# Kernel optimization log

Hardware: AMD Instinct MI355X
Metric: run time of the kernel (lower is better)

Reference implementation:

```python
import jax, jax.numpy as jnp
import numpy as np

N_HEAD = 16
D = 1024
LV = 2048
HEAD_DIM = D // N_HEAD
B = 2
LQ = 2048
LN_EPS = 1e-5


def setup_inputs() -> dict:
    key = jax.random.key(0)
    ks = jax.random.split(key, 8)
    s = 0.02
    v = jax.random.normal(ks[0], (B, LV, D), dtype=jnp.float32)
    q = jax.random.normal(ks[1], (B, LQ, D), dtype=jnp.float32)
    # per-head attn linear: d -> lv
    Wa = jax.random.normal(ks[2], (N_HEAD, D, LV), dtype=jnp.float32) * s
    ba = jnp.zeros((N_HEAD, LV), dtype=jnp.float32)
    # per-head layernorm over d
    gamma = jnp.ones((N_HEAD, D), dtype=jnp.float32)
    beta = jnp.zeros((N_HEAD, D), dtype=jnp.float32)
    # per-head proj (FilteredLinear modeled as affine): d -> head_dim
    Wp = jax.random.normal(ks[3], (N_HEAD, D, HEAD_DIM), dtype=jnp.float32) * s
    bp = jnp.zeros((N_HEAD, HEAD_DIM), dtype=jnp.float32)
    return {"v": v, "q": q, "Wa": Wa, "ba": ba, "gamma": gamma,
            "beta": beta, "Wp": Wp, "bp": bp}


def _mha(v, q, Wa, ba, gamma, beta, Wp, bp):
    # attn: [H, B, Lq, Lv] = relu(q @ Wa_h + ba_h)  (batched across heads)
    attn = jax.nn.relu(jnp.einsum('bqd,hdl->hbql', q, Wa)
                       + ba[:, None, None, :])
    # external-attention aggregation: [H, B, Lq, D]
    agg = jnp.einsum('hbql,bld->hbqd', attn, v)
    # per-head LayerNorm over last dim (d)
    mu = jnp.mean(agg, axis=-1, keepdims=True)
    var = jnp.var(agg, axis=-1, keepdims=True)
    normed = (agg - mu) * jax.lax.rsqrt(var + LN_EPS)
    normed = normed * gamma[:, None, None, :] + beta[:, None, None, :]
    # per-head projection to head_dim: [H, B, Lq, head_dim]
    heads = jnp.einsum('hbqd,hde->hbqe', normed, Wp) + bp[:, None, None, :]
    # concat heads along feature dim -> [B, Lq, D]
    return heads.transpose(1, 2, 0, 3).reshape(q.shape[0], q.shape[1], -1)


def reference(v, q, Wa, ba, gamma, beta, Wp, bp):
    return _mha(v, q, Wa, ba, gamma, beta, Wp, bp)
```

## Files before the change

### kernel.cpp

```cpp
#include <hip/hip_runtime.h>
#include <hip/hip_bf16.h>

typedef __attribute__((ext_vector_type(8))) short short8;
typedef __attribute__((ext_vector_type(4))) float f32x4;

#define N_HEAD 16
#define DMODEL 1024
#define LV 2048
#define LQ 2048
#define BATCH 2
#define HEAD_DIM 64

template <int N> struct IC { static constexpr int v = N; };

__device__ inline ushort f2bf(float f) {
    union { float f; unsigned u; } v; v.f = f;
    unsigned r = v.u + 0x7fffu + ((v.u >> 16) & 1u);
    return (ushort)(r >> 16);
}
__device__ inline float bf2f(ushort h) {
    union { unsigned u; float f; } v; v.u = ((unsigned)h) << 16;
    return v.f;
}

__global__ __launch_bounds__(256) void cast_bf16(const float* __restrict__ src,
                                                 ushort* __restrict__ dst, int n) {
    int i = (blockIdx.x * 256 + threadIdx.x) * 4;
    if (i < n) {
        float4 v = *(const float4*)(src + i);
        ushort4 o;
        o.x = f2bf(v.x); o.y = f2bf(v.y); o.z = f2bf(v.z); o.w = f2bf(v.w);
        *(ushort4*)(dst + i) = o;
    }
}

__global__ __launch_bounds__(256) void transpose_cast(const float* __restrict__ src,
                                                      ushort* __restrict__ dst,
                                                      int R, int C) {
    __shared__ float t[32][33];
    size_t zoff = (size_t)blockIdx.z * R * C;
    int c0 = blockIdx.x * 32, r0 = blockIdx.y * 32;
    int tx = threadIdx.x, ty = threadIdx.y;
#pragma unroll
    for (int i = 0; i < 4; ++i)
        t[ty + i * 8][tx] = src[zoff + (size_t)(r0 + ty + i * 8) * C + c0 + tx];
    __syncthreads();
#pragma unroll
    for (int i = 0; i < 4; ++i)
        dst[zoff + (size_t)(c0 + ty + i * 8) * R + r0 + tx] = f2bf(t[tx][ty + i * 8]);
}

template <bool RELU, int LNBN, int ZSH>
__global__ __launch_bounds__(512, 4) void gemm128x256(
    const ushort* __restrict__ A, const ushort* __restrict__ B,
    ushort* __restrict__ Cout, const float* __restrict__ bias,
    int K,
    long sA_b, long sA_h, long sB_b, long sB_h, long sC_z, int ldc, long sBias_h)
{
    __shared__ __align__(16) char smem[3 * 24576];

    const int gid = blockIdx.x;
    const int per = (int)gridDim.x >> 3;
    const int w = (gid & 7) * per + (gid >> 3);
    const int z = w >> ZSH;
    const int rem = w & ((1 << ZSH) - 1);
    const int bm0 = (rem >> LNBN) * 128;
    const int bn0 = (rem & ((1 << LNBN) - 1)) * 256;

    const int b = z & 1, h = z >> 1;
    A += (size_t)b * sA_b + (size_t)h * sA_h;
    B += (size_t)b * sB_b + (size_t)h * sB_h;
    const float* biasp = bias ? bias + (size_t)h * sBias_h : nullptr;

    const int T = threadIdx.x;
    const int lane = T & 63, wid = T >> 6;
    const int wr = wid >> 2, wc = wid & 3;
    const int fr = lane & 15, fq = lane >> 4;
    const int laneoff = fr * 64 + ((fq * 16) ^ ((fr >> 3) << 5));

    const int s_row = T >> 2;
    const int s_csw = ((T & 3) * 16) ^ (((T >> 5) & 1) << 5);
    const ushort* gA = A + (size_t)(bm0 + s_row) * K + (s_csw >> 1);
    const ushort* gB = B + (size_t)(bn0 + s_row) * K + (s_csw >> 1);

    const int nt = K >> 5;

    auto stage = [&](int sb, int kt) {
        char* base = smem + sb * 24576;
        const ushort* srcA = gA + (size_t)kt * 32;
        __builtin_amdgcn_global_load_lds(
            (const __attribute__((address_space(1))) void*)srcA,
            (__attribute__((address_space(3))) void*)(base + (T << 4)), 16, 0, 0);
#pragma unroll
        for (int j = 0; j < 2; ++j) {
            const ushort* srcB = gB + (size_t)j * 128 * K + (size_t)kt * 32;
            __builtin_amdgcn_global_load_lds(
                (const __attribute__((address_space(1))) void*)srcB,
                (__attribute__((address_space(3))) void*)(base + 8192 + j * 8192 + (T << 4)),
                16, 0, 0);
        }
    };

    f32x4 acc[4][4];
#pragma unroll
    for (int m = 0; m < 4; ++m)
#pragma unroll
        for (int n = 0; n < 4; ++n)
#pragma unroll
            for (int j = 0; j < 4; ++j) acc[m][n][j] = 0.f;

    auto step = [&](int t, int rb, int sb, auto DOST, auto VM) {
        const char* base = smem + rb * 24576;
        const char* pA = base + wr * 4096 + laneoff;
        const char* pB = base + 8192 + wc * 4096 + laneoff;
        short8 a[4], bb[4];
#pragma unroll
        for (int m = 0; m < 4; ++m) a[m] = *(const short8*)(pA + m * 1024);
#pragma unroll
        for (int n = 0; n < 4; ++n) bb[n] = *(const short8*)(pB + n * 1024);
        if constexpr (decltype(DOST)::v) stage(sb, t + 2);
        asm volatile("s_waitcnt lgkmcnt(0)" ::: "memory");
        __builtin_amdgcn_sched_barrier(0);
        __builtin_amdgcn_s_setprio(1);
#pragma unroll
        for (int m = 0; m < 4; ++m)
#pragma unroll
            for (int n = 0; n < 4; ++n)
                acc[m][n] = __builtin_amdgcn_mfma_f32_16x16x32_bf16(
                    a[m], bb[n], acc[m][n], 0, 0, 0);
        __builtin_amdgcn_s_setprio(0);
        __builtin_amdgcn_sched_barrier(0);
        constexpr int vm = decltype(VM)::v;
        if constexpr (vm == 3) asm volatile("s_waitcnt vmcnt(3)" ::: "memory");
        else if constexpr (vm == 0) asm volatile("s_waitcnt vmcnt(0)" ::: "memory");
        if constexpr (vm >= 0) asm volatile("s_barrier" ::: "memory");
    };

    stage(0, 0); stage(1, 1);
    asm volatile("s_waitcnt vmcnt(3)" ::: "memory");
    asm volatile("s_barrier" ::: "memory");

    int rb = 0, sb = 2;
    for (int t = 0; t < nt - 2; ++t) {
        step(t, rb, sb, IC<1>{}, IC<3>{});
        rb = (rb == 2) ? 0 : rb + 1;
        sb = (sb == 2) ? 0 : sb + 1;
    }
    step(nt - 2, rb, sb, IC<0>{}, IC<0>{});
    rb = (rb == 2) ? 0 : rb + 1;
    step(nt - 1, rb, sb, IC<0>{}, IC<-1>{});

    asm volatile("s_waitcnt vmcnt(0) lgkmcnt(0)" ::: "memory");
    __builtin_amdgcn_s_barrier();
    char* eb = smem + wid * 9216;
    const int row0 = bm0 + wr * 64;
    const int col0 = bn0 + wc * 64;
#pragma unroll
    for (int n = 0; n < 4; ++n) {
        const float bvv = biasp ? biasp[col0 + n * 16 + fr] : 0.f;
#pragma unroll
        for (int m = 0; m < 4; ++m) {
#pragma unroll
            for (int j = 0; j < 4; ++j) {
                float val = acc[m][n][j] + bvv;
                if (RELU) val = fmaxf(val, 0.f);
                *(ushort*)(eb + (m * 16 + fq * 4 + j) * 144 + (n * 16 + fr) * 2) = f2bf(val);
            }
        }
    }
    asm volatile("s_waitcnt lgkmcnt(0)" ::: "memory");
    ushort* C = Cout + (size_t)z * sC_z;
    const int rl = lane >> 3, cb = lane & 7;
#pragma unroll
    for (int i = 0; i < 8; ++i) {
        short8 vv = *(const short8*)(eb + (i * 8 + rl) * 144 + cb * 16);
        *(short8*)(C + (size_t)(row0 + i * 8 + rl) * ldc + col0 + cb * 8) = vv;
    }
}

__global__ __launch_bounds__(256) void lnproj_kernel(const ushort* __restrict__ agg,
                                                     const ushort* __restrict__ WpT,
                                                     const float* __restrict__ gamma,
                                                     const float* __restrict__ beta,
                                                     const float* __restrict__ bp,
                                                     float* __restrict__ out,
                                                     int h_base) {
    const int z = blockIdx.y, b = z & 1, hg = h_base + (z >> 1);
    const int wid = threadIdx.x >> 6, lane = threadIdx.x & 63;
    const int fr = lane & 15, fq = lane >> 4;
    const int m0 = (blockIdx.x * 4 + wid) * 16;

    const ushort* Arow = agg + ((size_t)z * 2048 + m0 + fr) * 1024 + fq * 8;

    float s = 0.f, s2 = 0.f;
    for (int kt = 0; kt < 32; ++kt) {
        short8 a = *(const short8*)(Arow + kt * 32);
#pragma unroll
        for (int j = 0; j < 8; ++j) { float x = bf2f((ushort)a[j]); s += x; s2 += x * x; }
    }
    s  += __shfl_xor(s, 16, 64);  s2 += __shfl_xor(s2, 16, 64);
    s  += __shfl_xor(s, 32, 64);  s2 += __shfl_xor(s2, 32, 64);
    const float mu  = s * (1.0f / 1024.0f);
    const float var = s2 * (1.0f / 1024.0f) - mu * mu;
    const float rs  = rsqrtf(fmaxf(var, 0.f) + 1e-5f);

    const ushort* Bbase = WpT + (size_t)hg * 64 * 1024 + (size_t)fr * 1024 + fq * 8;
    const float* gp = gamma + (size_t)hg * 1024 + fq * 8;
    const float* bt = beta  + (size_t)hg * 1024 + fq * 8;

    f32x4 acc[4];
#pragma unroll
    for (int n = 0; n < 4; ++n)
#pragma unroll
        for (int j = 0; j < 4; ++j) acc[n][j] = 0.f;

    for (int kt = 0; kt < 32; ++kt) {
        short8 a = *(const short8*)(Arow + kt * 32);
        float4 g0 = *(const float4*)(gp + kt * 32);
        float4 g1 = *(const float4*)(gp + kt * 32 + 4);
        float4 b0 = *(const float4*)(bt + kt * 32);
        float4 b1 = *(const float4*)(bt + kt * 32 + 4);
        const float gg[8] = {g0.x, g0.y, g0.z, g0.w, g1.x, g1.y, g1.z, g1.w};
        const float bb_[8] = {b0.x, b0.y, b0.z, b0.w, b1.x, b1.y, b1.z, b1.w};
        short8 an;
#pragma unroll
        for (int j = 0; j < 8; ++j) {
            float xn = (bf2f((ushort)a[j]) - mu) * rs * gg[j] + bb_[j];
            an[j] = (short)f2bf(xn);
        }
#pragma unroll
        for (int n = 0; n < 4; ++n) {
            short8 wv = *(const short8*)(Bbase + n * 16 * 1024 + kt * 32);
            acc[n] = __builtin_amdgcn_mfma_f32_16x16x32_bf16(an, wv, acc[n], 0, 0, 0);
        }
    }
#pragma unroll
    for (int n = 0; n < 4; ++n) {
        const int c = hg * 64 + n * 16 + fr;
        const float bvv = bp[c];
#pragma unroll
        for (int j = 0; j < 4; ++j)
            out[(size_t)b * 2048 * 1024 + (size_t)(m0 + fq * 4 + j) * 1024 + c] =
                acc[n][j] + bvv;
    }
}

extern "C" void kernel_launch(void* const* d_in, const int* in_sizes, int n_in,
                              void* d_out, int out_size, void* d_ws, size_t ws_size,
                              hipStream_t stream) {
    const float* v     = (const float*)d_in[0];
    const float* q     = (const float*)d_in[1];
    const float* Wa    = (const float*)d_in[2];
    const float* ba    = (const float*)d_in[3];
    const float* gamma = (const float*)d_in[4];
    const float* beta  = (const float*)d_in[5];
    const float* Wp    = (const float*)d_in[6];
    const float* bp    = (const float*)d_in[7];
    float* out = (float*)d_out;

    const size_t MB = 1ull << 20;
    char* ws = (char*)d_ws;
    ushort* qbf = (ushort*)(ws);
    ushort* vT  = (ushort*)(ws + 8 * MB);
    ushort* WpT = (ushort*)(ws + 16 * MB);
    int NH = 1;
    {
        const int cands[5] = {16, 8, 4, 2, 1};
        for (int i = 0; i < 5; ++i) {
            if ((size_t)(18 + 28 * cands[i]) * MB <= ws_size) { NH = cands[i]; break; }
        }
    }
    ushort* WaT_c  = (ushort*)(ws + 18 * MB);
    ushort* attn_c = (ushort*)(ws + (18 + (size_t)4 * NH) * MB);
    ushort* agg_c  = (ushort*)(ws + (18 + (size_t)20 * NH) * MB);

    dim3 tb(32, 8);
    cast_bf16<<<4096, 256, 0, stream>>>(q, qbf, BATCH * LQ * DMODEL);
    transpose_cast<<<dim3(DMODEL / 32, LV / 32, BATCH), tb, 0, stream>>>(v, vT, LV, DMODEL);
    transpose_cast<<<dim3(HEAD_DIM / 32, DMODEL / 32, N_HEAD), tb, 0, stream>>>(Wp, WpT, DMODEL, HEAD_DIM);

    for (int h0 = 0; h0 < N_HEAD; h0 += NH) {
        transpose_cast<<<dim3(LV / 32, DMODEL / 32, NH), tb, 0, stream>>>(
            Wa + (size_t)h0 * DMODEL * LV, WaT_c, DMODEL, LV);

        gemm128x256<true, 3, 7><<<128 * NH * 2, 512, 0, stream>>>(
            qbf, WaT_c, attn_c, ba + (size_t)h0 * LV, DMODEL,
            (long)LQ * DMODEL, 0L,
            0L, (long)LV * DMODEL,
            (long)LQ * LV, LV, (long)LV);

        gemm128x256<false, 2, 6><<<64 * NH * 2, 512, 0, stream>>>(
            attn_c, vT, agg_c, nullptr, LV,
            (long)LQ * LV, (long)2 * LQ * LV,
            (long)DMODEL * LV, 0L,
            (long)LQ * DMODEL, DMODEL, 0L);

        lnproj_kernel<<<dim3(LQ / 64, NH * 2), 256, 0, stream>>>(
            agg_c, WpT, gamma, beta, bp, out, h0);
    }
}
```

Before: 754.6 us.

## Use 4-wave 128x256 GEMM tiles with 128x64 per-wave subtiles and M-fast ordering

Halves the GEMM workgroup from 512 to 256 threads. Each wave now owns a full 128-row by 64-column output strip (8x4 MFMA accumulators) instead of 64x64, which raises register-level reuse of B fragments and cuts LDS reads per MFMA. Staging is redistributed so each thread issues six async global-to-LDS loads per k-tile, and the waitcnt thresholds are adjusted to match. The first GEMM also gets an M-fastest block ordering for better L2 reuse of the Wa tiles. The cost is higher register pressure (launch bounds 256,2) and fewer waves to hide latency.

```diff
diff --git a/kernel.cpp b/kernel.cpp
--- a/kernel.cpp
+++ b/kernel.cpp
@@ -50,8 +50,8 @@
         dst[zoff + (size_t)(c0 + ty + i * 8) * R + r0 + tx] = f2bf(t[tx][ty + i * 8]);
 }
 
-template <bool RELU, int LNBN, int ZSH>
-__global__ __launch_bounds__(512, 4) void gemm128x256(
+template <bool RELU, int LNA, int ZSH, bool BMFAST>
+__global__ __launch_bounds__(256, 2) void gemm128x256(
     const ushort* __restrict__ A, const ushort* __restrict__ B,
     ushort* __restrict__ Cout, const float* __restrict__ bias,
     int K,
@@ -64,8 +64,9 @@
     const int w = (gid & 7) * per + (gid >> 3);
     const int z = w >> ZSH;
     const int rem = w & ((1 << ZSH) - 1);
-    const int bm0 = (rem >> LNBN) * 128;
-    const int bn0 = (rem & ((1 << LNBN) - 1)) * 256;
+    int bm0, bn0;
+    if (BMFAST) { bm0 = (rem & ((1 << LNA) - 1)) * 128; bn0 = (rem >> LNA) * 256; }
+    else        { bn0 = (rem & ((1 << LNA) - 1)) * 256; bm0 = (rem >> LNA) * 128; }
 
     const int b = z & 1, h = z >> 1;
     A += (size_t)b * sA_b + (size_t)h * sA_h;
@@ -73,37 +74,40 @@
     const float* biasp = bias ? bias + (size_t)h * sBias_h : nullptr;
 
     const int T = threadIdx.x;
-    const int lane = T & 63, wid = T >> 6;
-    const int wr = wid >> 2, wc = wid & 3;
+    const int lane = T & 63, wc = T >> 6;
     const int fr = lane & 15, fq = lane >> 4;
     const int laneoff = fr * 64 + ((fq * 16) ^ ((fr >> 3) << 5));
 
-    const int s_row = T >> 2;
-    const int s_csw = ((T & 3) * 16) ^ (((T >> 5) & 1) << 5);
-    const ushort* gA = A + (size_t)(bm0 + s_row) * K + (s_csw >> 1);
-    const ushort* gB = B + (size_t)(bn0 + s_row) * K + (s_csw >> 1);
+    const int s_rowA = ((T >> 6) << 4) + ((T >> 2) & 15);
+    const int s_csw  = ((T & 3) * 16) ^ (((T >> 5) & 1) << 5);
+    const ushort* gA = A + (size_t)(bm0 + s_rowA) * K + (s_csw >> 1);
+    const ushort* gB = B + (size_t)(bn0 + s_rowA) * K + (s_csw >> 1);
 
     const int nt = K >> 5;
 
     auto stage = [&](int sb, int kt) {
         char* base = smem + sb * 24576;
-        const ushort* srcA = gA + (size_t)kt * 32;
-        __builtin_amdgcn_global_load_lds(
-            (const __attribute__((address_space(1))) void*)srcA,
-            (__attribute__((address_space(3))) void*)(base + (T << 4)), 16, 0, 0);
 #pragma unroll
         for (int j = 0; j < 2; ++j) {
-            const ushort* srcB = gB + (size_t)j * 128 * K + (size_t)kt * 32;
+            const ushort* src = gA + (size_t)j * 64 * K + (size_t)kt * 32;
             __builtin_amdgcn_global_load_lds(
-                (const __attribute__((address_space(1))) void*)srcB,
-                (__attribute__((address_space(3))) void*)(base + 8192 + j * 8192 + (T << 4)),
+                (const __attribute__((address_space(1))) void*)src,
+                (__attribute__((address_space(3))) void*)(base + j * 4096 + (T << 4)),
                 16, 0, 0);
         }
+#pragma unroll
+        for (int j = 0; j < 4; ++j) {
+            const ushort* src = gB + (size_t)j * 64 * K + (size_t)kt * 32;
+            __builtin_amdgcn_global_load_lds(
+                (const __attribute__((address_space(1))) void*)src,
+                (__attribute__((address_space(3))) void*)(base + 8192 + j * 4096 + (T << 4)),
+                16, 0, 0);
+        }
     };
 
-    f32x4 acc[4][4];
-#pragma unroll
-    for (int m = 0; m < 4; ++m)
+    f32x4 acc[8][4];
+#pragma unroll
+    for (int m = 0; m < 8; ++m)
 #pragma unroll
         for (int n = 0; n < 4; ++n)
 #pragma unroll
@@ -111,11 +115,11 @@
 
     auto step = [&](int t, int rb, int sb, auto DOST, auto VM) {
         const char* base = smem + rb * 24576;
-        const char* pA = base + wr * 4096 + laneoff;
+        const char* pA = base + laneoff;
         const char* pB = base + 8192 + wc * 4096 + laneoff;
-        short8 a[4], bb[4];
-#pragma unroll
-        for (int m = 0; m < 4; ++m) a[m] = *(const short8*)(pA + m * 1024);
+        short8 a[8], bb[4];
+#pragma unroll
+        for (int m = 0; m < 8; ++m) a[m] = *(const short8*)(pA + m * 1024);
 #pragma unroll
         for (int n = 0; n < 4; ++n) bb[n] = *(const short8*)(pB + n * 1024);
         if constexpr (decltype(DOST)::v) stage(sb, t + 2);
@@ -123,7 +127,7 @@
         __builtin_amdgcn_sched_barrier(0);
         __builtin_amdgcn_s_setprio(1);
 #pragma unroll
-        for (int m = 0; m < 4; ++m)
+        for (int m = 0; m < 8; ++m)
 #pragma unroll
             for (int n = 0; n < 4; ++n)
                 acc[m][n] = __builtin_amdgcn_mfma_f32_16x16x32_bf16(
@@ -131,18 +135,18 @@
         __builtin_amdgcn_s_setprio(0);
         __builtin_amdgcn_sched_barrier(0);
         constexpr int vm = decltype(VM)::v;
-        if constexpr (vm == 3) asm volatile("s_waitcnt vmcnt(3)" ::: "memory");
+        if constexpr (vm == 6) asm volatile("s_waitcnt vmcnt(6)" ::: "memory");
         else if constexpr (vm == 0) asm volatile("s_waitcnt vmcnt(0)" ::: "memory");
         if constexpr (vm >= 0) asm volatile("s_barrier" ::: "memory");
     };
 
     stage(0, 0); stage(1, 1);
-    asm volatile("s_waitcnt vmcnt(3)" ::: "memory");
+    asm volatile("s_waitcnt vmcnt(6)" ::: "memory");
     asm volatile("s_barrier" ::: "memory");
 
     int rb = 0, sb = 2;
     for (int t = 0; t < nt - 2; ++t) {
-        step(t, rb, sb, IC<1>{}, IC<3>{});
+        step(t, rb, sb, IC<1>{}, IC<6>{});
         rb = (rb == 2) ? 0 : rb + 1;
         sb = (sb == 2) ? 0 : sb + 1;
     }
@@ -152,14 +156,13 @@
 
     asm volatile("s_waitcnt vmcnt(0) lgkmcnt(0)" ::: "memory");
     __builtin_amdgcn_s_barrier();
-    char* eb = smem + wid * 9216;
-    const int row0 = bm0 + wr * 64;
+    char* eb = smem + wc * 18432;
     const int col0 = bn0 + wc * 64;
 #pragma unroll
     for (int n = 0; n < 4; ++n) {
         const float bvv = biasp ? biasp[col0 + n * 16 + fr] : 0.f;
 #pragma unroll
-        for (int m = 0; m < 4; ++m) {
+        for (int m = 0; m < 8; ++m) {
 #pragma unroll
             for (int j = 0; j < 4; ++j) {
                 float val = acc[m][n][j] + bvv;
@@ -172,9 +175,9 @@
     ushort* C = Cout + (size_t)z * sC_z;
     const int rl = lane >> 3, cb = lane & 7;
 #pragma unroll
-    for (int i = 0; i < 8; ++i) {
+    for (int i = 0; i < 16; ++i) {
         short8 vv = *(const short8*)(eb + (i * 8 + rl) * 144 + cb * 16);
-        *(short8*)(C + (size_t)(row0 + i * 8 + rl) * ldc + col0 + cb * 8) = vv;
+        *(short8*)(C + (size_t)(bm0 + i * 8 + rl) * ldc + col0 + cb * 8) = vv;
     }
 }
 
@@ -283,13 +286,13 @@
         transpose_cast<<<dim3(LV / 32, DMODEL / 32, NH), tb, 0, stream>>>(
             Wa + (size_t)h0 * DMODEL * LV, WaT_c, DMODEL, LV);
 
-        gemm128x256<true, 3, 7><<<128 * NH * 2, 512, 0, stream>>>(
+        gemm128x256<true, 4, 7, true><<<128 * NH * 2, 256, 0, stream>>>(
             qbf, WaT_c, attn_c, ba + (size_t)h0 * LV, DMODEL,
             (long)LQ * DMODEL, 0L,
             0L, (long)LV * DMODEL,
             (long)LQ * LV, LV, (long)LV);
 
-        gemm128x256<false, 2, 6><<<64 * NH * 2, 512, 0, stream>>>(
+        gemm128x256<false, 2, 6, false><<<64 * NH * 2, 256, 0, stream>>>(
             attn_c, vT, agg_c, nullptr, LV,
             (long)LQ * LV, (long)2 * LQ * LV,
             (long)DMODEL * LV, 0L,
```

Result: faster. 713.6 us (-5.4%).

## Deepen GEMM pipeline to 4 LDS stages with register double-buffered fragments

Applied to the files above, without the earlier changes.

The bf16 GEMM kernel moves from a 3-buffer to a 4-buffer LDS ring with prefetch distance 3. LDS fragment reads for the next k-step are double-buffered in registers and interleaved with the MFMAs through sched_group_barrier, so LDS latency hides behind matrix math. A template flag also reorders the tile walk so the first GEMM iterates M-fast, changing which tiles share the cache. The cost is more LDS and registers, so launch bounds drop to 2 blocks per CU, which lowers occupancy.

```diff
diff --git a/kernel.cpp b/kernel.cpp
--- a/kernel.cpp
+++ b/kernel.cpp
@@ -50,22 +50,23 @@
         dst[zoff + (size_t)(c0 + ty + i * 8) * R + r0 + tx] = f2bf(t[tx][ty + i * 8]);
 }
 
-template <bool RELU, int LNBN, int ZSH>
-__global__ __launch_bounds__(512, 4) void gemm128x256(
+template <bool RELU, int LNA, int ZSH, bool BMFAST>
+__global__ __launch_bounds__(512, 2) void gemm128x256(
     const ushort* __restrict__ A, const ushort* __restrict__ B,
     ushort* __restrict__ Cout, const float* __restrict__ bias,
     int K,
     long sA_b, long sA_h, long sB_b, long sB_h, long sC_z, int ldc, long sBias_h)
 {
-    __shared__ __align__(16) char smem[3 * 24576];
+    __shared__ __align__(16) char smem[4 * 24576];
 
     const int gid = blockIdx.x;
     const int per = (int)gridDim.x >> 3;
     const int w = (gid & 7) * per + (gid >> 3);
     const int z = w >> ZSH;
     const int rem = w & ((1 << ZSH) - 1);
-    const int bm0 = (rem >> LNBN) * 128;
-    const int bn0 = (rem & ((1 << LNBN) - 1)) * 256;
+    int bm0, bn0;
+    if (BMFAST) { bm0 = (rem & ((1 << LNA) - 1)) * 128; bn0 = (rem >> LNA) * 256; }
+    else        { bn0 = (rem & ((1 << LNA) - 1)) * 256; bm0 = (rem >> LNA) * 128; }
 
     const int b = z & 1, h = z >> 1;
     A += (size_t)b * sA_b + (size_t)h * sA_h;
@@ -85,8 +86,8 @@
 
     const int nt = K >> 5;
 
-    auto stage = [&](int sb, int kt) {
-        char* base = smem + sb * 24576;
+    auto stage = [&](int kt) {
+        char* base = smem + (kt & 3) * 24576;
         const ushort* srcA = gA + (size_t)kt * 32;
         __builtin_amdgcn_global_load_lds(
             (const __attribute__((address_space(1))) void*)srcA,
@@ -101,54 +102,63 @@
         }
     };
 
-    f32x4 acc[4][4];
-#pragma unroll
-    for (int m = 0; m < 4; ++m)
-#pragma unroll
-        for (int n = 0; n < 4; ++n)
-#pragma unroll
-            for (int j = 0; j < 4; ++j) acc[m][n][j] = 0.f;
-
-    auto step = [&](int t, int rb, int sb, auto DOST, auto VM) {
-        const char* base = smem + rb * 24576;
+    struct Frag { short8 a[4], bb[4]; };
+    auto ldfrag = [&](int kt, Frag& F) {
+        const char* base = smem + (kt & 3) * 24576;
         const char* pA = base + wr * 4096 + laneoff;
         const char* pB = base + 8192 + wc * 4096 + laneoff;
-        short8 a[4], bb[4];
-#pragma unroll
-        for (int m = 0; m < 4; ++m) a[m] = *(const short8*)(pA + m * 1024);
-#pragma unroll
-        for (int n = 0; n < 4; ++n) bb[n] = *(const short8*)(pB + n * 1024);
-        if constexpr (decltype(DOST)::v) stage(sb, t + 2);
-        asm volatile("s_waitcnt lgkmcnt(0)" ::: "memory");
-        __builtin_amdgcn_sched_barrier(0);
+#pragma unroll
+        for (int m = 0; m < 4; ++m) F.a[m] = *(const short8*)(pA + m * 1024);
+#pragma unroll
+        for (int n = 0; n < 4; ++n) F.bb[n] = *(const short8*)(pB + n * 1024);
+    };
+
+    f32x4 acc[4][4];
+#pragma unroll
+    for (int m = 0; m < 4; ++m)
+#pragma unroll
+        for (int n = 0; n < 4; ++n)
+#pragma unroll
+            for (int j = 0; j < 4; ++j) acc[m][n][j] = 0.f;
+
+    auto step = [&](int t, Frag& rd, Frag& mm, auto DOST, auto DORD, auto VM) {
+        if constexpr (decltype(DOST)::v) stage(t + 3);
+        if constexpr (decltype(DORD)::v) ldfrag(t + 1, rd);
         __builtin_amdgcn_s_setprio(1);
 #pragma unroll
         for (int m = 0; m < 4; ++m)
 #pragma unroll
             for (int n = 0; n < 4; ++n)
                 acc[m][n] = __builtin_amdgcn_mfma_f32_16x16x32_bf16(
-                    a[m], bb[n], acc[m][n], 0, 0, 0);
+                    mm.a[m], mm.bb[n], acc[m][n], 0, 0, 0);
         __builtin_amdgcn_s_setprio(0);
-        __builtin_amdgcn_sched_barrier(0);
+        if constexpr (decltype(DORD)::v) {
+#pragma unroll
+            for (int g = 0; g < 4; ++g) {
+                __builtin_amdgcn_sched_group_barrier(0x100, 2, 0);
+                __builtin_amdgcn_sched_group_barrier(0x008, 4, 0);
+            }
+        }
         constexpr int vm = decltype(VM)::v;
         if constexpr (vm == 3) asm volatile("s_waitcnt vmcnt(3)" ::: "memory");
         else if constexpr (vm == 0) asm volatile("s_waitcnt vmcnt(0)" ::: "memory");
         if constexpr (vm >= 0) asm volatile("s_barrier" ::: "memory");
     };
 
-    stage(0, 0); stage(1, 1);
+    stage(0); stage(1); stage(2);
     asm volatile("s_waitcnt vmcnt(3)" ::: "memory");
     asm volatile("s_barrier" ::: "memory");
-
-    int rb = 0, sb = 2;
-    for (int t = 0; t < nt - 2; ++t) {
-        step(t, rb, sb, IC<1>{}, IC<3>{});
-        rb = (rb == 2) ? 0 : rb + 1;
-        sb = (sb == 2) ? 0 : sb + 1;
-    }
-    step(nt - 2, rb, sb, IC<0>{}, IC<0>{});
-    rb = (rb == 2) ? 0 : rb + 1;
-    step(nt - 1, rb, sb, IC<0>{}, IC<-1>{});
+    Frag f0, f1;
+    ldfrag(0, f0);
+
+    for (int t = 0; t < nt - 4; t += 2) {
+        step(t,     f1, f0, IC<1>{}, IC<1>{}, IC<3>{});
+        step(t + 1, f0, f1, IC<1>{}, IC<1>{}, IC<3>{});
+    }
+    step(nt - 4, f1, f0, IC<1>{}, IC<1>{}, IC<3>{});
+    step(nt - 3, f0, f1, IC<0>{}, IC<1>{}, IC<0>{});
+    step(nt - 2, f1, f0, IC<0>{}, IC<1>{}, IC<-1>{});
+    step(nt - 1, f0, f1, IC<0>{}, IC<0>{}, IC<-1>{});
 
     asm volatile("s_waitcnt vmcnt(0) lgkmcnt(0)" ::: "memory");
     __builtin_amdgcn_s_barrier();
@@ -283,13 +293,13 @@
         transpose_cast<<<dim3(LV / 32, DMODEL / 32, NH), tb, 0, stream>>>(
             Wa + (size_t)h0 * DMODEL * LV, WaT_c, DMODEL, LV);
 
-        gemm128x256<true, 3, 7><<<128 * NH * 2, 512, 0, stream>>>(
+        gemm128x256<true, 4, 7, true><<<128 * NH * 2, 512, 0, stream>>>(
             qbf, WaT_c, attn_c, ba + (size_t)h0 * LV, DMODEL,
             (long)LQ * DMODEL, 0L,
             0L, (long)LV * DMODEL,
             (long)LQ * LV, LV, (long)LV);
 
-        gemm128x256<false, 2, 6><<<64 * NH * 2, 512, 0, stream>>>(
+        gemm128x256<false, 2, 6, false><<<64 * NH * 2, 512, 0, stream>>>(
             attn_c, vT, agg_c, nullptr, LV,
             (long)LQ * LV, (long)2 * LQ * LV,
             (long)DMODEL * LV, 0L,
```

Result: slower. 849.1 us (+12.5%).
